# Kernel optimization log

Measured on AMD Instinct MI355X. Metric: run time of the kernel, lower is better.

The kernel has to match this reference:

```python
import jax, jax.numpy as jnp
import numpy as np

B = 131072
N_CONF = 512
N_REP = 256            # n_confounder_rep == n_outcome_rep
N_TREAT = 64           # 2 ** n_cause, n_cause = 6
COMBINED = 2 * N_REP   # 512


def _mlp_params(key, d_in, d_hid, d_out, scale=0.02):
    k1, k2, k3, k4 = jax.random.split(key, 4)
    return (jax.random.normal(k1, (d_hid, d_in), jnp.float32) * scale,
            jax.random.normal(k2, (d_hid,), jnp.float32) * scale,
            jax.random.normal(k3, (d_out, d_hid), jnp.float32) * scale,
            jax.random.normal(k4, (d_out,), jnp.float32) * scale)


def setup_inputs() -> dict:
    key = jax.random.key(0)
    kx, kc, k1, k2, k3, kh = jax.random.split(key, 6)
    x = jax.random.normal(kx, (B, N_CONF), jnp.float32)
    cause = jax.random.randint(kc, (B,), 0, N_TREAT, jnp.int64 if jax.config.jax_enable_x64 else jnp.int32)
    W1c, b1c, W2c, b2c = _mlp_params(k1, N_CONF, N_CONF + 1, N_REP)
    W1o, b1o, W2o, b2o = _mlp_params(k2, N_CONF, N_CONF + 1, N_REP)
    W1p, b1p, W2p, b2p = _mlp_params(k3, N_REP, N_REP + 1, N_TREAT)
    kh1, kh2 = jax.random.split(kh)
    Wh = jax.random.normal(kh1, (N_TREAT, COMBINED), jnp.float32) * 0.02  # stacked heads
    bh = jax.random.normal(kh2, (N_TREAT,), jnp.float32) * 0.02
    return {"x": x, "cause": cause,
            "W1c": W1c, "b1c": b1c, "W2c": W2c, "b2c": b2c,
            "W1o": W1o, "b1o": b1o, "W2o": W2o, "b2o": b2o,
            "W1p": W1p, "b1p": b1p, "W2p": W2p, "b2p": b2p,
            "Wh": Wh, "bh": bh}


def _mlp(x, W1, b1, W2, b2):
    h = jax.nn.relu(x @ W1.T + b1)
    return h @ W2.T + b2


def reference(x, cause, W1c, b1c, W2c, b2c, W1o, b1o, W2o, b2o,
              W1p, b1p, W2p, b2p, Wh, bh):
    confounder_rep = _mlp(x, W1c, b1c, W2c, b2c)              # [B, N_REP]
    outcome_rep = _mlp(x, W1o, b1o, W2o, b2o)                 # [B, N_REP]
    combined = jnp.concatenate([confounder_rep, outcome_rep], axis=-1)  # [B, 2*N_REP]
    # dense multi-head prediction: all N_TREAT heads, then one-hot select
    prediction = combined @ Wh.T + bh                          # [B, N_TREAT]
    cause_mat = jax.nn.one_hot(cause, N_TREAT, dtype=prediction.dtype)
    prediction_selected = jnp.sum(prediction * cause_mat, axis=1, keepdims=True)  # [B, 1]
    logits = _mlp(confounder_rep, W1p, b1p, W2p, b2p)          # [B, N_TREAT]
    log_propensity = jax.nn.log_softmax(logits, axis=-1)
    mmd = jnp.float32(0.0)  # lam_mmd == 0.0 path
    return prediction_selected, log_propensity, mmd, cause
```

## Files before the change

### kernel.cpp

```cpp
#include <hip/hip_runtime.h>


typedef __attribute__((ext_vector_type(8))) short bf16x8;
typedef __attribute__((ext_vector_type(4))) float f32x4;
typedef __attribute__((ext_vector_type(4))) short s16x4;

#define MFMA16 __builtin_amdgcn_mfma_f32_16x16x32_bf16

__device__ __forceinline__ short f2bf(float f) {
  union { float f; unsigned u; } v; v.f = f;
  return (short)((v.u + 0x7FFFu + ((v.u >> 16) & 1u)) >> 16);
}

__global__ void prep_weights(const float* __restrict__ W1c, const float* __restrict__ W2c,
                             const float* __restrict__ W1o, const float* __restrict__ W2o,
                             const float* __restrict__ W1p, const float* __restrict__ W2p,
                             const float* __restrict__ Wh,
                             const float* __restrict__ b1c, const float* __restrict__ b1o,
                             const float* __restrict__ b1p,
                             char* __restrict__ ws) {
  int s = blockIdx.x * 256 + threadIdx.x;
  if (s < 960512) {
    float v;
    if (s < 278528)      { int n = s >> 9,        k = s & 511;        v = (n < 513) ? W1c[n * 512 + k] : 0.f; }
    else if (s < 417792) { int i = s - 278528; int n = i / 544, k = i - n * 544; v = (k < 513) ? W2c[n * 513 + k] : 0.f; }
    else if (s < 696320) { int i = s - 417792; int n = i >> 9,  k = i & 511;     v = (n < 513) ? W1o[n * 512 + k] : 0.f; }
    else if (s < 835584) { int i = s - 696320; int n = i / 544, k = i - n * 544; v = (k < 513) ? W2o[n * 513 + k] : 0.f; }
    else if (s < 909312) { int i = s - 835584; int n = i >> 8,  k = i & 255;     v = (n < 257) ? W1p[n * 256 + k] : 0.f; }
    else if (s < 927744) { int i = s - 909312; int n = i / 288, k = i - n * 288; v = (k < 257) ? W2p[n * 257 + k] : 0.f; }
    else                 { v = Wh[s - 927744]; }
    ((short*)ws)[s] = f2bf(v);
  } else if (s < 961888) {
    int j = s - 960512;
    float v;
    if (j < 544)       v = (j < 513) ? b1c[j] : 0.f;
    else if (j < 1088) { int q = j - 544;  v = (q < 513) ? b1o[q] : 0.f; }
    else               { int q = j - 1088; v = (q < 257) ? b1p[q] : 0.f; }
    ((float*)(ws + 1921024))[j] = v;
  }
}

template<int NKT, int NRG>
__device__ __forceinline__ void pair_mm(const short* __restrict__ W, int ldw,
                                        const short* __restrict__ A, int lda,
                                        int nt0, int rg0, int l15, int l4,
                                        f32x4 (&acc0)[NRG], f32x4 (&acc1)[NRG]) {
  bf16x8 b0[NKT], b1[NKT];
  const short* w0 = W + (nt0 * 16 + l15) * ldw + l4 * 8;
  const short* w1 = w0 + 16 * ldw;
  #pragma unroll
  for (int kt = 0; kt < NKT; ++kt) {
    b0[kt] = *(const bf16x8*)(w0 + kt * 32);
    b1[kt] = *(const bf16x8*)(w1 + kt * 32);
  }
  #pragma unroll
  for (int g = 0; g < NRG; ++g) {
    acc0[g] = (f32x4){0.f, 0.f, 0.f, 0.f};
    acc1[g] = (f32x4){0.f, 0.f, 0.f, 0.f};
  }
  #pragma unroll
  for (int kt = 0; kt < NKT; ++kt) {
    #pragma unroll
    for (int g = 0; g < NRG; ++g) {
      bf16x8 a = *(const bf16x8*)(A + ((rg0 + g) * 16 + l15) * lda + kt * 32 + l4 * 8);
      acc0[g] = MFMA16(a, b0[kt], acc0[g], 0, 0, 0);
      acc1[g] = MFMA16(a, b1[kt], acc1[g], 0, 0, 0);
    }
  }
}

template<int NRG>
__device__ __forceinline__ void store_tile(short* __restrict__ dst, int ldd, int nt,
                                           const float* __restrict__ bias,
                                           const f32x4 (&acc)[NRG], int rg0,
                                           int l15, int l4, bool relu) {
  float bi = bias[nt * 16 + l15];
  #pragma unroll
  for (int g = 0; g < NRG; ++g)
    #pragma unroll
    for (int r = 0; r < 4; ++r) {
      float v = acc[g][r] + bi;
      if (relu) v = fmaxf(v, 0.f);
      dst[((rg0 + g) * 16 + l4 * 4 + r) * ldd + nt * 16 + l15] = f2bf(v);
    }
}

__global__ __launch_bounds__(1024, 4)
void fused_main(const float* __restrict__ x, const int* __restrict__ cause,
                const char* __restrict__ ws,
                const float* __restrict__ b2c, const float* __restrict__ b2o,
                const float* __restrict__ b2p, const float* __restrict__ bh,
                float* __restrict__ out) {
  const short* W1cb = (const short*)(ws);
  const short* W2cb = (const short*)(ws + 557056);
  const short* W1ob = (const short*)(ws + 835584);
  const short* W2ob = (const short*)(ws + 1392640);
  const short* W1pb = (const short*)(ws + 1671168);
  const short* W2pb = (const short*)(ws + 1818624);
  const short* Whb  = (const short*)(ws + 1855488);
  const float* b1cp = (const float*)(ws + 1921024);
  const float* b1op = (const float*)(ws + 1923200);
  const float* b1pp = (const float*)(ws + 1925376);

  extern __shared__ __align__(16) char lds[];
  short* Cs    = (short*)lds;
  short* Os    = (short*)(lds + 33792);
  short* Hs    = (short*)(lds + 67584);
  short* Xs    = (short*)lds;
  float* headB = (float*)(lds + 67584);
  short* Hp    = (short*)(lds + 67584);

  const int tid  = threadIdx.x;
  const int lane = tid & 63;
  const int wid  = tid >> 6;
  const int l15  = lane & 15;
  const int l4   = lane >> 4;
  const size_t grow0 = (size_t)blockIdx.x * 64;

  {
    const f32x4* xsrc = (const f32x4*)(x + grow0 * 512);
    for (int i = tid; i < 8192; i += 1024) {
      f32x4 v = __builtin_nontemporal_load(xsrc + i);
      int r = i >> 7, c = i & 127;
      s16x4 p;
      p.x = f2bf(v.x); p.y = f2bf(v.y); p.z = f2bf(v.z); p.w = f2bf(v.w);
      *(s16x4*)&Xs[r * 520 + c * 4] = p;
    }
  }
  __syncthreads();

  for (int p = wid; p < 17; p += 16) {
    f32x4 a0[4], a1[4];
    pair_mm<16, 4>(W1cb, 512, Xs, 520, 2 * p, 0, l15, l4, a0, a1);
    store_tile<4>(Hs, 552, 2 * p,     b1cp, a0, 0, l15, l4, true);
    store_tile<4>(Hs, 552, 2 * p + 1, b1cp, a1, 0, l15, l4, true);
  }
  __syncthreads();

  const int p2 = wid >> 1;
  const int h2 = (wid & 1) * 2;
  s16x4 crp[2][2];
  {
    f32x4 a0[2], a1[2];
    pair_mm<17, 2>(W2cb, 544, Hs, 552, 2 * p2, h2, l15, l4, a0, a1);
    float bi0 = b2c[p2 * 32 + l15], bi1 = b2c[p2 * 32 + 16 + l15];
    #pragma unroll
    for (int g = 0; g < 2; ++g) {
      s16x4 q0, q1;
      #pragma unroll
      for (int r = 0; r < 4; ++r) {
        q0[r] = f2bf(a0[g][r] + bi0);
        q1[r] = f2bf(a1[g][r] + bi1);
      }
      crp[0][g] = q0; crp[1][g] = q1;
    }
  }
  __syncthreads();

  for (int p = (wid + 8) & 15; p < 17; p += 16) {
    f32x4 a0[4], a1[4];
    pair_mm<16, 4>(W1ob, 512, Xs, 520, 2 * p, 0, l15, l4, a0, a1);
    store_tile<4>(Hs, 552, 2 * p,     b1op, a0, 0, l15, l4, true);
    store_tile<4>(Hs, 552, 2 * p + 1, b1op, a1, 0, l15, l4, true);
  }
  __syncthreads();

  #pragma unroll
  for (int jj = 0; jj < 2; ++jj) {
    int nt = 2 * p2 + jj;
    #pragma unroll
    for (int g = 0; g < 2; ++g)
      #pragma unroll
      for (int r = 0; r < 4; ++r)
        Cs[((h2 + g) * 16 + l4 * 4 + r) * 264 + nt * 16 + l15] = crp[jj][g][r];
  }

  {
    f32x4 a0[2], a1[2];
    pair_mm<17, 2>(W2ob, 544, Hs, 552, 2 * p2, h2, l15, l4, a0, a1);
    store_tile<2>(Os, 264, 2 * p2,     b2o, a0, h2, l15, l4, false);
    store_tile<2>(Os, 264, 2 * p2 + 1, b2o, a1, h2, l15, l4, false);
  }
  __syncthreads();

  {
    const int g  = wid >> 2;
    const int j  = wid & 3;
    const int rb = g * 16;
    bf16x8 acf[16];
    #pragma unroll
    for (int kt = 0; kt < 8; ++kt) {
      acf[kt]     = *(const bf16x8*)&Cs[(rb + l15) * 264 + kt * 32 + l4 * 8];
      acf[kt + 8] = *(const bf16x8*)&Os[(rb + l15) * 264 + kt * 32 + l4 * 8];
    }
    f32x4 hacc = {0.f, 0.f, 0.f, 0.f};
    const short* w0 = Whb + (j * 16 + l15) * 512 + l4 * 8;
    #pragma unroll
    for (int kt = 0; kt < 16; ++kt)
      hacc = MFMA16(acf[kt], *(const bf16x8*)(w0 + kt * 32), hacc, 0, 0, 0);
    #pragma unroll
    for (int r = 0; r < 4; ++r)
      headB[(rb + l4 * 4 + r) * 68 + j * 16 + l15] = hacc[r];
  }
  __syncthreads();

  if (wid < 4 && lane < 16) {
    int row = wid * 16 + lane;
    size_t gr = grow0 + row;
    int cv = cause[gr];
    out[gr] = headB[row * 68 + cv] + bh[cv];
    out[(size_t)8519681 + gr] = (float)cv;
  }
  __syncthreads();

  for (int q = (wid + 4) & 15; q < 18; q += 16) {
    int pp = q >> 1, hh = (q & 1) * 2;
    f32x4 a0[2], a1[2];
    pair_mm<8, 2>(W1pb, 256, Cs, 264, 2 * pp, hh, l15, l4, a0, a1);
    store_tile<2>(Hp, 296, 2 * pp,     b1pp, a0, hh, l15, l4, true);
    store_tile<2>(Hp, 296, 2 * pp + 1, b1pp, a1, hh, l15, l4, true);
  }
  __syncthreads();

  if (wid < 4) {
    const int rb = wid * 16;
    f32x4 pl[4];
    {
      bf16x8 ahp[9];
      #pragma unroll
      for (int kt = 0; kt < 9; ++kt)
        ahp[kt] = *(const bf16x8*)&Hp[(rb + l15) * 296 + kt * 32 + l4 * 8];
      #pragma unroll
      for (int nt = 0; nt < 4; ++nt) {
        f32x4 a0 = {0.f, 0.f, 0.f, 0.f};
        const short* w0 = W2pb + (nt * 16 + l15) * 288 + l4 * 8;
        #pragma unroll
        for (int kt = 0; kt < 9; ++kt)
          a0 = MFMA16(ahp[kt], *(const bf16x8*)(w0 + kt * 32), a0, 0, 0, 0);
        float bi = b2p[nt * 16 + l15];
        #pragma unroll
        for (int r = 0; r < 4; ++r) a0[r] += bi;
        pl[nt] = a0;
      }
    }
    #pragma unroll
    for (int r = 0; r < 4; ++r) {
      float m = fmaxf(fmaxf(pl[0][r], pl[1][r]), fmaxf(pl[2][r], pl[3][r]));
      m = fmaxf(m, __shfl_xor(m, 1, 64));
      m = fmaxf(m, __shfl_xor(m, 2, 64));
      m = fmaxf(m, __shfl_xor(m, 4, 64));
      m = fmaxf(m, __shfl_xor(m, 8, 64));
      float s = __expf(pl[0][r] - m) + __expf(pl[1][r] - m)
              + __expf(pl[2][r] - m) + __expf(pl[3][r] - m);
      s += __shfl_xor(s, 1, 64);
      s += __shfl_xor(s, 2, 64);
      s += __shfl_xor(s, 4, 64);
      s += __shfl_xor(s, 8, 64);
      float lse = m + __logf(s);
      size_t gr = grow0 + rb + l4 * 4 + r;
      float* o1 = out + 131072 + gr * 64;
      #pragma unroll
      for (int nt = 0; nt < 4; ++nt)
        o1[nt * 16 + l15] = pl[nt][r] - lse;
    }
  }
  if (blockIdx.x == 0 && tid == 0) out[8519680] = 0.0f;
}

extern "C" void kernel_launch(void* const* d_in, const int* in_sizes, int n_in,
                              void* d_out, int out_size, void* d_ws, size_t ws_size,
                              hipStream_t stream) {
  (void)in_sizes; (void)n_in; (void)out_size; (void)ws_size;
  const float* x    = (const float*)d_in[0];
  const int*   cause= (const int*)  d_in[1];
  const float* W1c  = (const float*)d_in[2];
  const float* b1c  = (const float*)d_in[3];
  const float* W2c  = (const float*)d_in[4];
  const float* b2c  = (const float*)d_in[5];
  const float* W1o  = (const float*)d_in[6];
  const float* b1o  = (const float*)d_in[7];
  const float* W2o  = (const float*)d_in[8];
  const float* b2o  = (const float*)d_in[9];
  const float* W1p  = (const float*)d_in[10];
  const float* b1p  = (const float*)d_in[11];
  const float* W2p  = (const float*)d_in[12];
  const float* b2p  = (const float*)d_in[13];
  const float* Wh   = (const float*)d_in[14];
  const float* bh   = (const float*)d_in[15];
  char* ws = (char*)d_ws;

  prep_weights<<<3758, 256, 0, stream>>>(W1c, W2c, W1o, W2o, W1p, W2p, Wh,
                                         b1c, b1o, b1p, ws);

  (void)hipFuncSetAttribute((const void*)fused_main,
                            hipFuncAttributeMaxDynamicSharedMemorySize, 138240);
  fused_main<<<2048, 1024, 138240, stream>>>(x, cause, ws, b2c, b2o, b2p, bh,
                                             (float*)d_out);
}
```

Before: 640.1 us.

## Halve block row tile and swizzle LDS layout to remove padding

Each block now handles 32 rows with 512 threads instead of 64 rows with 1024 threads, and twice as many blocks are launched. Shared memory drops from 138 KB to 69 KB, so more blocks can be resident per CU. Padded LDS strides are replaced by an XOR swizzle on 8-element groups to avoid bank conflicts. The cost is that each block loads the weight fragments from global or L2 for only half as many rows, so weight traffic per row doubles.

```diff
diff --git a/kernel.cpp b/kernel.cpp
--- a/kernel.cpp
+++ b/kernel.cpp
@@ -10,6 +10,14 @@
 __device__ __forceinline__ short f2bf(float f) {
   union { float f; unsigned u; } v; v.f = f;
   return (short)((v.u + 0x7FFFu + ((v.u >> 16) & 1u)) >> 16);
+}
+
+__device__ __forceinline__ const bf16x8* ldsRd8(const short* base, int row,
+                                                int grp, int LD) {
+  return (const bf16x8*)(base + row * LD + ((grp ^ (row & 7)) << 3));
+}
+__device__ __forceinline__ short* ldsPtr(short* base, int row, int col, int LD) {
+  return base + row * LD + ((((col >> 3) ^ (row & 7)) << 3) | (col & 7));
 }
 
 __global__ void prep_weights(const float* __restrict__ W1c, const float* __restrict__ W2c,
@@ -62,7 +70,7 @@
   for (int kt = 0; kt < NKT; ++kt) {
     #pragma unroll
     for (int g = 0; g < NRG; ++g) {
-      bf16x8 a = *(const bf16x8*)(A + ((rg0 + g) * 16 + l15) * lda + kt * 32 + l4 * 8);
+      bf16x8 a = *ldsRd8(A, (rg0 + g) * 16 + l15, kt * 4 + l4, lda);
       acc0[g] = MFMA16(a, b0[kt], acc0[g], 0, 0, 0);
       acc1[g] = MFMA16(a, b1[kt], acc1[g], 0, 0, 0);
     }
@@ -81,11 +89,11 @@
     for (int r = 0; r < 4; ++r) {
       float v = acc[g][r] + bi;
       if (relu) v = fmaxf(v, 0.f);
-      dst[((rg0 + g) * 16 + l4 * 4 + r) * ldd + nt * 16 + l15] = f2bf(v);
-    }
-}
-
-__global__ __launch_bounds__(1024, 4)
+      *ldsPtr(dst, (rg0 + g) * 16 + l4 * 4 + r, nt * 16 + l15, ldd) = f2bf(v);
+    }
+}
+
+__global__ __launch_bounds__(512, 4)
 void fused_main(const float* __restrict__ x, const int* __restrict__ cause,
                 const char* __restrict__ ws,
                 const float* __restrict__ b2c, const float* __restrict__ b2o,
@@ -104,46 +112,45 @@
 
   extern __shared__ __align__(16) char lds[];
   short* Cs    = (short*)lds;
-  short* Os    = (short*)(lds + 33792);
-  short* Hs    = (short*)(lds + 67584);
+  short* Os    = (short*)(lds + 16384);
+  short* Hs    = (short*)(lds + 32768);
   short* Xs    = (short*)lds;
-  float* headB = (float*)(lds + 67584);
-  short* Hp    = (short*)(lds + 67584);
+  float* headB = (float*)(lds + 32768);
+  short* Hp    = (short*)(lds + 32768);
 
   const int tid  = threadIdx.x;
   const int lane = tid & 63;
   const int wid  = tid >> 6;
   const int l15  = lane & 15;
   const int l4   = lane >> 4;
-  const size_t grow0 = (size_t)blockIdx.x * 64;
+  const size_t grow0 = (size_t)blockIdx.x * 32;
 
   {
     const f32x4* xsrc = (const f32x4*)(x + grow0 * 512);
-    for (int i = tid; i < 8192; i += 1024) {
+    for (int i = tid; i < 4096; i += 512) {
       f32x4 v = __builtin_nontemporal_load(xsrc + i);
       int r = i >> 7, c = i & 127;
       s16x4 p;
       p.x = f2bf(v.x); p.y = f2bf(v.y); p.z = f2bf(v.z); p.w = f2bf(v.w);
-      *(s16x4*)&Xs[r * 520 + c * 4] = p;
-    }
-  }
-  __syncthreads();
-
-  for (int p = wid; p < 17; p += 16) {
-    f32x4 a0[4], a1[4];
-    pair_mm<16, 4>(W1cb, 512, Xs, 520, 2 * p, 0, l15, l4, a0, a1);
-    store_tile<4>(Hs, 552, 2 * p,     b1cp, a0, 0, l15, l4, true);
-    store_tile<4>(Hs, 552, 2 * p + 1, b1cp, a1, 0, l15, l4, true);
-  }
-  __syncthreads();
-
-  const int p2 = wid >> 1;
-  const int h2 = (wid & 1) * 2;
+      int grp = (c >> 1) ^ (r & 7);
+      *(s16x4*)(Xs + r * 512 + (grp << 3) + ((c & 1) << 2)) = p;
+    }
+  }
+  __syncthreads();
+
+  for (int p = wid; p < 17; p += 8) {
+    f32x4 a0[2], a1[2];
+    pair_mm<16, 2>(W1cb, 512, Xs, 512, 2 * p, 0, l15, l4, a0, a1);
+    store_tile<2>(Hs, 576, 2 * p,     b1cp, a0, 0, l15, l4, true);
+    store_tile<2>(Hs, 576, 2 * p + 1, b1cp, a1, 0, l15, l4, true);
+  }
+  __syncthreads();
+
   s16x4 crp[2][2];
   {
     f32x4 a0[2], a1[2];
-    pair_mm<17, 2>(W2cb, 544, Hs, 552, 2 * p2, h2, l15, l4, a0, a1);
-    float bi0 = b2c[p2 * 32 + l15], bi1 = b2c[p2 * 32 + 16 + l15];
+    pair_mm<17, 2>(W2cb, 544, Hs, 576, 2 * wid, 0, l15, l4, a0, a1);
+    float bi0 = b2c[wid * 32 + l15], bi1 = b2c[wid * 32 + 16 + l15];
     #pragma unroll
     for (int g = 0; g < 2; ++g) {
       s16x4 q0, q1;
@@ -157,29 +164,29 @@
   }
   __syncthreads();
 
-  for (int p = (wid + 8) & 15; p < 17; p += 16) {
-    f32x4 a0[4], a1[4];
-    pair_mm<16, 4>(W1ob, 512, Xs, 520, 2 * p, 0, l15, l4, a0, a1);
-    store_tile<4>(Hs, 552, 2 * p,     b1op, a0, 0, l15, l4, true);
-    store_tile<4>(Hs, 552, 2 * p + 1, b1op, a1, 0, l15, l4, true);
+  for (int p = 7 - wid; p < 17; p += 8) {
+    f32x4 a0[2], a1[2];
+    pair_mm<16, 2>(W1ob, 512, Xs, 512, 2 * p, 0, l15, l4, a0, a1);
+    store_tile<2>(Hs, 576, 2 * p,     b1op, a0, 0, l15, l4, true);
+    store_tile<2>(Hs, 576, 2 * p + 1, b1op, a1, 0, l15, l4, true);
   }
   __syncthreads();
 
   #pragma unroll
   for (int jj = 0; jj < 2; ++jj) {
-    int nt = 2 * p2 + jj;
+    int nt = 2 * wid + jj;
     #pragma unroll
     for (int g = 0; g < 2; ++g)
       #pragma unroll
       for (int r = 0; r < 4; ++r)
-        Cs[((h2 + g) * 16 + l4 * 4 + r) * 264 + nt * 16 + l15] = crp[jj][g][r];
+        *ldsPtr(Cs, g * 16 + l4 * 4 + r, nt * 16 + l15, 256) = crp[jj][g][r];
   }
 
   {
     f32x4 a0[2], a1[2];
-    pair_mm<17, 2>(W2ob, 544, Hs, 552, 2 * p2, h2, l15, l4, a0, a1);
-    store_tile<2>(Os, 264, 2 * p2,     b2o, a0, h2, l15, l4, false);
-    store_tile<2>(Os, 264, 2 * p2 + 1, b2o, a1, h2, l15, l4, false);
+    pair_mm<17, 2>(W2ob, 544, Hs, 576, 2 * wid, 0, l15, l4, a0, a1);
+    store_tile<2>(Os, 256, 2 * wid,     b2o, a0, 0, l15, l4, false);
+    store_tile<2>(Os, 256, 2 * wid + 1, b2o, a1, 0, l15, l4, false);
   }
   __syncthreads();
 
@@ -190,8 +197,8 @@
     bf16x8 acf[16];
     #pragma unroll
     for (int kt = 0; kt < 8; ++kt) {
-      acf[kt]     = *(const bf16x8*)&Cs[(rb + l15) * 264 + kt * 32 + l4 * 8];
-      acf[kt + 8] = *(const bf16x8*)&Os[(rb + l15) * 264 + kt * 32 + l4 * 8];
+      acf[kt]     = *ldsRd8(Cs, rb + l15, kt * 4 + l4, 256);
+      acf[kt + 8] = *ldsRd8(Os, rb + l15, kt * 4 + l4, 256);
     }
     f32x4 hacc = {0.f, 0.f, 0.f, 0.f};
     const short* w0 = Whb + (j * 16 + l15) * 512 + l4 * 8;
@@ -204,7 +211,7 @@
   }
   __syncthreads();
 
-  if (wid < 4 && lane < 16) {
+  if (wid < 2 && lane < 16) {
     int row = wid * 16 + lane;
     size_t gr = grow0 + row;
     int cv = cause[gr];
@@ -213,23 +220,22 @@
   }
   __syncthreads();
 
-  for (int q = (wid + 4) & 15; q < 18; q += 16) {
-    int pp = q >> 1, hh = (q & 1) * 2;
-    f32x4 a0[2], a1[2];
-    pair_mm<8, 2>(W1pb, 256, Cs, 264, 2 * pp, hh, l15, l4, a0, a1);
-    store_tile<2>(Hp, 296, 2 * pp,     b1pp, a0, hh, l15, l4, true);
-    store_tile<2>(Hp, 296, 2 * pp + 1, b1pp, a1, hh, l15, l4, true);
-  }
-  __syncthreads();
-
-  if (wid < 4) {
+  for (int p = wid; p < 9; p += 8) {
+    f32x4 a0[2], a1[2];
+    pair_mm<8, 2>(W1pb, 256, Cs, 256, 2 * p, 0, l15, l4, a0, a1);
+    store_tile<2>(Hp, 320, 2 * p,     b1pp, a0, 0, l15, l4, true);
+    store_tile<2>(Hp, 320, 2 * p + 1, b1pp, a1, 0, l15, l4, true);
+  }
+  __syncthreads();
+
+  if (wid < 2) {
     const int rb = wid * 16;
     f32x4 pl[4];
     {
       bf16x8 ahp[9];
       #pragma unroll
       for (int kt = 0; kt < 9; ++kt)
-        ahp[kt] = *(const bf16x8*)&Hp[(rb + l15) * 296 + kt * 32 + l4 * 8];
+        ahp[kt] = *ldsRd8(Hp, rb + l15, kt * 4 + l4, 320);
       #pragma unroll
       for (int nt = 0; nt < 4; ++nt) {
         f32x4 a0 = {0.f, 0.f, 0.f, 0.f};
@@ -293,7 +299,7 @@
                                          b1c, b1o, b1p, ws);
 
   (void)hipFuncSetAttribute((const void*)fused_main,
-                            hipFuncAttributeMaxDynamicSharedMemorySize, 138240);
-  fused_main<<<2048, 1024, 138240, stream>>>(x, cause, ws, b2c, b2o, b2p, bh,
-                                             (float*)d_out);
-}
+                            hipFuncAttributeMaxDynamicSharedMemorySize, 69632);
+  fused_main<<<4096, 512, 69632, stream>>>(x, cause, ws, b2c, b2o, b2p, bh,
+                                           (float*)d_out);
+}
```

Result: slower. 935.2 us (+46.1%).
